# Kernel optimization log

Measured on AMD Instinct MI355X. Metric: run time of the kernel, lower is better.

## Reference

```python
import jax, jax.numpy as jnp
import numpy as np

_COOR = [[1,4],[1,5],[1,6],[2,4],[2,6],[3,1],[3,2],[3,3],[3,4],[3,5],[3,6],[3,7],[3,8],[3,9],[4,1],[4,2],[4,3],[4,4],[4,5],[4,6],[4,7],[4,8],[4,9],[5,1],[5,2],[5,3],[5,4],[5,5],[5,6],[5,7],[5,8],[5,9],[6,1],[6,2],[6,3],[6,4],[6,5],[6,6],[6,7],[6,8],[6,9],[7,1],[7,2],[7,3],[7,4],[7,5],[7,6],[7,7],[7,8],[7,9],[8,2],[8,3],[8,4],[8,5],[8,6],[8,7],[8,8],[9,3],[9,4],[9,5],[9,6],[9,7]]
_DIRS = [[1,2,3,4,5,6,7,8,9,10,11,12,13,14,15,16,17,18,19,20,21,22,23,24,25,26,27,28,29,30,31,32,33,34,35,36,37,38,39,40,41,42,43,44,45,46,47,48,49,50,58,52,53,54,55,56,62,60,61,51,57,59],[59,57,51,61,60,62,56,55,54,53,52,58,50,41,32,23,14,49,40,31,22,13,48,39,30,21,12,47,38,29,20,11,46,37,28,19,10,45,36,27,18,9,44,35,26,17,8,43,34,25,16,7,42,33,24,15,6,5,4,3,2,1],[59,57,51,61,60,62,56,55,54,53,52,58,50,49,48,47,46,45,44,43,42,41,40,39,38,37,36,35,34,33,32,31,30,29,28,27,26,25,24,23,22,21,20,19,18,17,16,15,14,13,12,11,10,9,8,7,6,5,4,3,2,1],[1,2,3,4,5,6,15,24,33,42,7,16,25,34,43,8,17,26,35,44,9,18,27,36,45,10,19,28,37,46,11,20,29,38,47,12,21,30,39,48,13,22,31,40,49,14,23,32,41,50,58,52,53,54,55,56,62,60,61,51,57,59]]


def _build_graph():
    D, E = len(_DIRS), len(_COOR)
    Ns = np.zeros((D, E, E), np.float32)
    for di, direction in enumerate(_DIRS):
        for pi in range(E):
            i, j = _COOR[direction[pi] - 1]
            nbrs = {0: [[i, j - 1], [i - 1, j - 1], [i - 1, j]],
                    1: [[i, j + 1], [i - 1, j], [i - 1, j + 1]],
                    2: [[i, j - 1], [i + 1, j - 1], [i + 1, j]],
                    3: [[i, j - 1], [i - 1, j - 1], [i - 1, j]]}[di]
            for nb in nbrs:
                if nb in _COOR:
                    n_idx = _COOR.index(nb) + 1
                    if n_idx in direction[:pi]:
                        Ns[di, pi, direction.index(n_idx)] = 1.0
    perm = np.asarray(_DIRS, np.int32) - 1  # [D,E] electrode index visited at each step
    return jnp.asarray(Ns), jnp.asarray(perm)


def _srnn(x_t, Ns, perm, U_w, U_b, W_w, W_b, sp_bs, P_w, P_b, ps_w, ps_b):
    # x_t: [B,E,C] -> m: [B,HID]
    B, E, _ = x_t.shape
    HID = U_b.shape[1]

    def one_dir(ns, pm, uw, ub, ww, wb, b, pw, pb):
        ux = jnp.einsum('bec,hc->beh', x_t[:, pm], uw) + ub  # [B,E,H] precomputed input term
        H0 = jnp.zeros((B, E, ub.shape[0]), x_t.dtype)

        def step(H, inp):
            ns_row, ux_pi, pi = inp
            # ns_row is nonzero only at already-visited step positions (< pi)
            h_agg = jnp.einsum('e,beh->bh', ns_row, H)
            h = jax.nn.relu(ux_pi + h_agg @ ww.T + wb + b)
            return jax.lax.dynamic_update_slice(H, h[:, None, :], (0, pi, 0)), None

        H, _ = jax.lax.scan(step, H0, (ns, jnp.swapaxes(ux, 0, 1), jnp.arange(E)))
        return jnp.einsum('beh,pe->bhp', H, pw) + pb  # [B,H,P]

    s = jax.vmap(one_dir)(Ns, perm, U_w, U_b, W_w, W_b, sp_bs, P_w, P_b)  # [D,B,H,P]
    s = jnp.moveaxis(s, 0, 2).reshape(B, HID, -1)  # [B,H,D*P]
    return (s @ ps_w.T + ps_b)[..., 0]  # [B,H]


def _trnn(ms, rs_w, rs_b, vs_w, vs_b, bs, pj_w, pj_b):
    # ms: [T,B,H]
    h0 = jnp.zeros(ms.shape[1:], ms.dtype)

    def step(h, m_t):
        h = jax.nn.relu(m_t @ rs_w.T + rs_b + h @ vs_w.T + vs_b + bs)
        return h, h

    _, hs = jax.lax.scan(step, h0, ms)  # [T,B,H]
    return jnp.einsum('tbh,pt->bph', hs, pj_w) + pj_b[None, :, None]  # [B,P,H]


def _forward(x, Ns, perm, U_w, U_b, W_w, W_b, sp_bs, P_w, P_b, ps_w, ps_b,
             f_rs_w, f_rs_b, f_vs_w, f_vs_b, f_bs, f_pj_w, f_pj_b,
             b_rs_w, b_rs_b, b_vs_w, b_vs_b, b_bs, b_pj_w, b_pj_b,
             fp1_w, fp1_b, fp2_w, fp2_b, bp1_w, bp1_b, bp2_w, bp2_b):
    xt = jnp.swapaxes(x, 0, 1)  # [T,B,E,C]
    ms = jax.vmap(lambda xi: _srnn(xi, Ns, perm, U_w, U_b, W_w, W_b, sp_bs,
                                   P_w, P_b, ps_w, ps_b))(xt)  # [T,B,H]
    q_f = _trnn(ms, f_rs_w, f_rs_b, f_vs_w, f_vs_b, f_bs, f_pj_w, f_pj_b)
    q_b = _trnn(ms[::-1], b_rs_w, b_rs_b, b_vs_w, b_vs_b, b_bs, b_pj_w, b_pj_b)
    zf = (q_f @ fp1_w.T + fp1_b)[..., 0]  # [B,Ptp]
    zb = (q_b @ bp1_w.T + bp1_b)[..., 0]
    return zf @ fp2_w.T + fp2_b + zb @ bp2_w.T + bp2_b  # [B,classes]


def setup_inputs() -> dict:
    B, T, E, C = 128, 16, 62, 5
    HID, SPP, TPP, NC, D = 128, 16, 8, 3, 4
    Ns, perm = _build_graph()
    key = jax.random.key(0)
    ks = jax.random.split(key, 34)
    rnd = lambda k, s: (jax.random.normal(k, s, jnp.float32) * 0.05)
    return {
        'x': jax.random.normal(ks[0], (B, T, E, C), jnp.float32),
        'Ns': Ns, 'perm': perm,
        'U_w': rnd(ks[1], (D, HID, C)), 'U_b': rnd(ks[2], (D, HID)),
        'W_w': rnd(ks[3], (D, HID, HID)), 'W_b': rnd(ks[4], (D, HID)),
        'sp_bs': rnd(ks[5], (D, HID)),
        'P_w': rnd(ks[6], (D, SPP, E)), 'P_b': rnd(ks[7], (D, SPP)),
        'ps_w': rnd(ks[8], (1, D * SPP)), 'ps_b': rnd(ks[9], (1,)),
        'f_rs_w': rnd(ks[10], (HID, HID)), 'f_rs_b': rnd(ks[11], (HID,)),
        'f_vs_w': rnd(ks[12], (HID, HID)), 'f_vs_b': rnd(ks[13], (HID,)),
        'f_bs': rnd(ks[14], (HID,)),
        'f_pj_w': rnd(ks[15], (TPP, T)), 'f_pj_b': rnd(ks[16], (TPP,)),
        'b_rs_w': rnd(ks[17], (HID, HID)), 'b_rs_b': rnd(ks[18], (HID,)),
        'b_vs_w': rnd(ks[19], (HID, HID)), 'b_vs_b': rnd(ks[20], (HID,)),
        'b_bs': rnd(ks[21], (HID,)),
        'b_pj_w': rnd(ks[22], (TPP, T)), 'b_pj_b': rnd(ks[23], (TPP,)),
        'fp1_w': rnd(ks[24], (1, HID)), 'fp1_b': rnd(ks[25], (1,)),
        'fp2_w': rnd(ks[26], (NC, TPP)), 'fp2_b': rnd(ks[27], (NC,)),
        'bp1_w': rnd(ks[28], (1, HID)), 'bp1_b': rnd(ks[29], (1,)),
        'bp2_w': rnd(ks[30], (NC, TPP)), 'bp2_b': rnd(ks[31], (NC,)),
    }


def reference(x, Ns, perm, U_w, U_b, W_w, W_b, sp_bs, P_w, P_b, ps_w, ps_b,
              f_rs_w, f_rs_b, f_vs_w, f_vs_b, f_bs, f_pj_w, f_pj_b,
              b_rs_w, b_rs_b, b_vs_w, b_vs_b, b_bs, b_pj_w, b_pj_b,
              fp1_w, fp1_b, fp2_w, fp2_b, bp1_w, bp1_b, bp2_w, bp2_b):
    return _forward(x, Ns, perm, U_w, U_b, W_w, W_b, sp_bs, P_w, P_b, ps_w, ps_b,
                    f_rs_w, f_rs_b, f_vs_w, f_vs_b, f_bs, f_pj_w, f_pj_b,
                    b_rs_w, b_rs_b, b_vs_w, b_vs_b, b_bs, b_pj_w, b_pj_b,
                    fp1_w, fp1_b, fp2_w, fp2_b, bp1_w, bp1_b, bp2_w, bp2_b)
```

## Files before the change

kernel.cpp:

```cpp
#include <hip/hip_runtime.h>
#include <utility>

typedef unsigned short u16;
typedef unsigned int   u32;

using bf16x8 = __attribute__((ext_vector_type(8))) short;
using f32x4  = __attribute__((ext_vector_type(4))) float;
using u32x4  = __attribute__((ext_vector_type(4))) unsigned;

__device__ __forceinline__ u32 cvtpk(float lo, float hi) {
  u32 r;
  asm("v_cvt_pk_bf16_f32 %0, %1, %2" : "=v"(r) : "v"(lo), "v"(hi));
  return r;
}
__device__ __forceinline__ bf16x8 pack8(float f0,float f1,float f2,float f3,
                                        float f4,float f5,float f6,float f7) {
  u32x4 t; t[0]=cvtpk(f0,f1); t[1]=cvtpk(f2,f3); t[2]=cvtpk(f4,f5); t[3]=cvtpk(f6,f7);
  return __builtin_bit_cast(bf16x8, t);
}
__device__ __forceinline__ u16 f2bf(float f) {
  u32 u = __float_as_uint(f);
  u32 r = u + 0x7FFFu + ((u >> 16) & 1u);
  return (u16)(r >> 16);
}

struct Sched {
  unsigned v[4][64];
  unsigned char opi[4][64];
  int nslot;
};

constexpr int cCOOR[62][2] = {
  {1,4},{1,5},{1,6},{2,4},{2,6},
  {3,1},{3,2},{3,3},{3,4},{3,5},{3,6},{3,7},{3,8},{3,9},
  {4,1},{4,2},{4,3},{4,4},{4,5},{4,6},{4,7},{4,8},{4,9},
  {5,1},{5,2},{5,3},{5,4},{5,5},{5,6},{5,7},{5,8},{5,9},
  {6,1},{6,2},{6,3},{6,4},{6,5},{6,6},{6,7},{6,8},{6,9},
  {7,1},{7,2},{7,3},{7,4},{7,5},{7,6},{7,7},{7,8},{7,9},
  {8,2},{8,3},{8,4},{8,5},{8,6},{8,7},{8,8},
  {9,3},{9,4},{9,5},{9,6},{9,7}};

constexpr int cDIRS[4][62] = {
  {1,2,3,4,5,6,7,8,9,10,11,12,13,14,15,16,17,18,19,20,21,22,23,24,25,26,27,28,29,30,
   31,32,33,34,35,36,37,38,39,40,41,42,43,44,45,46,47,48,49,50,
   58,52,53,54,55,56,62,60,61,51,57,59},
  {59,57,51,61,60,62,56,55,54,53,52,58,50,41,32,23,14,49,40,31,22,13,48,39,30,21,12,
   47,38,29,20,11,46,37,28,19,10,45,36,27,18,9,44,35,26,17,8,43,34,25,16,7,42,33,24,
   15,6,5,4,3,2,1},
  {59,57,51,61,60,62,56,55,54,53,52,58,50,49,48,47,46,45,44,43,42,41,40,39,38,37,36,
   35,34,33,32,31,30,29,28,27,26,25,24,23,22,21,20,19,18,17,16,15,14,13,12,11,10,9,
   8,7,6,5,4,3,2,1},
  {1,2,3,4,5,6,15,24,33,42,7,16,25,34,43,8,17,26,35,44,9,18,27,36,45,10,19,28,37,46,
   11,20,29,38,47,12,21,30,39,48,13,22,31,40,49,14,23,32,41,50,
   58,52,53,54,55,56,62,60,61,51,57,59}};

constexpr int cOFFS[4][3][2] = {
  {{0,-1},{-1,-1},{-1,0}},
  {{0, 1},{-1, 0},{-1,1}},
  {{0,-1},{ 1,-1},{ 1,0}},
  {{0,-1},{-1,-1},{-1,0}}};

constexpr Sched make_sched() {
  Sched S{};
  int nslot_all = 0;
  for (int d = 0; d < 4; ++d) {
    int pos_of[63] = {};
    for (int p = 0; p < 62; ++p) pos_of[cDIRS[d][p]] = p;
    int nb[62][3] = {}; int nc[62] = {}; int rdcnt[62] = {};
    for (int p = 0; p < 62; ++p) {
      const int e = cDIRS[d][p];
      const int ci = cCOOR[e-1][0], cj = cCOOR[e-1][1];
      for (int o = 0; o < 3; ++o) {
        const int ni = ci + cOFFS[d][o][0], nj = cj + cOFFS[d][o][1];
        int q = 0;
        for (int k2 = 0; k2 < 62; ++k2)
          if (cCOOR[k2][0]==ni && cCOOR[k2][1]==nj) { q = k2+1; break; }
        if (q) { const int qp = pos_of[q];
          if (qp < p) { nb[p][nc[p]] = qp; nc[p] = nc[p]+1; rdcnt[qp] = rdcnt[qp]+1; } }
      }
    }
    int lvl[62] = {};
    for (int p = 0; p < 62; ++p) {
      int m = 0;
      for (int o = 0; o < nc[p]; ++o) if (lvl[nb[p][o]] > m) m = lvl[nb[p][o]];
      lvl[p] = m + 1;
    }
    int ord[62] = {}; int k = 0;
    for (int L = 1; L <= 62; ++L)
      for (int p = 0; p < 62; ++p) if (lvl[p] == L) { ord[k] = p; k = k+1; }
    int slotof[62] = {};
    int rl[20]; int lr[20];
    for (int s = 0; s < 20; ++s) { rl[s] = 0; lr[s] = -1; }
    int nslot = 0, cur_sub = 0;
    int barafter[62] = {};
    int prev_lvl = lvl[ord[0]];
    for (int kk = 0; kk < 62; ++kk) {
      const int p = ord[kk];
      if (lvl[p] != prev_lvl) { barafter[kk-1] = 1; cur_sub = cur_sub+1; prev_lvl = lvl[p]; }
      for (int o = 0; o < nc[p]; ++o) {
        const int s = slotof[nb[p][o]];
        rl[s] = rl[s]-1;
        if (cur_sub > lr[s]) lr[s] = cur_sub;
      }
      int myslot = 31;
      if (rdcnt[p] > 0) {
        int found = -1;
        for (int s = 0; s < nslot; ++s)
          if (rl[s] == 0 && lr[s] < cur_sub) { found = s; break; }
        if (found < 0 && nslot < 19) { found = nslot; nslot = nslot+1; }
        if (found < 0) {
          barafter[kk-1] = 1; cur_sub = cur_sub+1;
          for (int o = 0; o < nc[p]; ++o) {
            const int s = slotof[nb[p][o]];
            if (cur_sub > lr[s]) lr[s] = cur_sub;
          }
          for (int s = 0; s < nslot; ++s)
            if (rl[s] == 0 && lr[s] < cur_sub) { found = s; break; }
        }
        if (found < 0 && nslot < 20) { found = nslot; nslot = nslot+1; }
        if (found < 0) found = 0;
        myslot = found;
        rl[myslot] = rdcnt[p];
        lr[myslot] = -1;
        slotof[p] = myslot;
      }
      S.opi[d][kk] = (unsigned char)p;
      S.v[d][kk] = (unsigned)(cDIRS[d][p]-1)
                 | ((unsigned)myslot << 6)
                 | ((unsigned)nc[p] << 11)
                 | ((unsigned)(nc[p]>0 ? slotof[nb[p][0]] : 0) << 13)
                 | ((unsigned)(nc[p]>1 ? slotof[nb[p][1]] : 0) << 18)
                 | ((unsigned)(nc[p]>2 ? slotof[nb[p][2]] : 0) << 23);
    }
    for (int kk = 0; kk < 62; ++kk) if (barafter[kk]) S.v[d][kk] |= (1u << 28);
    if (nslot > nslot_all) nslot_all = nslot;
  }
  S.nslot = nslot_all;
  return S;
}

constexpr Sched g_sched = make_sched();
static_assert(g_sched.nslot >= 8 && g_sched.nslot <= 20, "slot pressure out of range");
__constant__ Sched c_sched = make_sched();

constexpr int POOL_B    = g_sched.nslot * 4096;
constexpr int SRNN_SMEM = POOL_B + 256;

template <int D, int K>
__device__ __forceinline__ void do_step(
    char* smem, const float* s_wp,
    const bf16x8 (&wf)[2][4], const bf16x8& uwf0, const bf16x8& uwf1,
    float bias0, float bias1,
    const u32 (&xr)[16][3], const int (&bad)[4],
    const u32 (&rdv)[4], const u32 (&wav)[4],
    f32x4& macc0, f32x4& macc1)
{
  constexpr unsigned sv = g_sched.v[D][K];
  constexpr int snew = (int)((sv >> 6) & 31u);
  constexpr int nbc  = (int)((sv >> 11) & 3u);
  constexpr int sl0  = (int)((sv >> 13) & 31u);
  constexpr int sl1  = (int)((sv >> 18) & 31u);
  constexpr int sl2  = (int)((sv >> 23) & 31u);
  constexpr int g    = K & 3;
  constexpr int js   = K >> 2;

  u32 r0 = (u32)__builtin_amdgcn_ds_bpermute(bad[g], (int)xr[js][0]);
  u32 r1 = (u32)__builtin_amdgcn_ds_bpermute(bad[g], (int)xr[js][1]);
  u32 r2 = (u32)__builtin_amdgcn_ds_bpermute(bad[g], (int)xr[js][2]);

  f32x4 a0 = {bias0, bias0, bias0, bias0};
  f32x4 a1 = {bias1, bias1, bias1, bias1};

  if constexpr (nbc > 0) {
#pragma unroll
    for (int kc = 0; kc < 4; ++kc) {
      bf16x8 a = *(const bf16x8*)(smem + sl0 * 4096 + rdv[kc]);
      a0 = __builtin_amdgcn_mfma_f32_16x16x32_bf16(a, wf[0][kc], a0, 0, 0, 0);
      a1 = __builtin_amdgcn_mfma_f32_16x16x32_bf16(a, wf[1][kc], a1, 0, 0, 0);
    }
  }
  if constexpr (nbc > 1) {
#pragma unroll
    for (int kc = 0; kc < 4; ++kc) {
      bf16x8 a = *(const bf16x8*)(smem + sl1 * 4096 + rdv[kc]);
      a0 = __builtin_amdgcn_mfma_f32_16x16x32_bf16(a, wf[0][kc], a0, 0, 0, 0);
      a1 = __builtin_amdgcn_mfma_f32_16x16x32_bf16(a, wf[1][kc], a1, 0, 0, 0);
    }
  }
  if constexpr (nbc > 2) {
#pragma unroll
    for (int kc = 0; kc < 4; ++kc) {
      bf16x8 a = *(const bf16x8*)(smem + sl2 * 4096 + rdv[kc]);
      a0 = __builtin_amdgcn_mfma_f32_16x16x32_bf16(a, wf[0][kc], a0, 0, 0, 0);
      a1 = __builtin_amdgcn_mfma_f32_16x16x32_bf16(a, wf[1][kc], a1, 0, 0, 0);
    }
  }
  {
    u32x4 xv; xv[0] = r0; xv[1] = r1; xv[2] = r2; xv[3] = 0;
    bf16x8 xa = __builtin_bit_cast(bf16x8, xv);
    a0 = __builtin_amdgcn_mfma_f32_16x16x32_bf16(xa, uwf0, a0, 0, 0, 0);
    a1 = __builtin_amdgcn_mfma_f32_16x16x32_bf16(xa, uwf1, a1, 0, 0, 0);
  }

  const float wp = s_wp[K];
  float h0[4], h1[4];
#pragma unroll
  for (int r = 0; r < 4; ++r) { h0[r] = fmaxf(a0[r], 0.f); h1[r] = fmaxf(a1[r], 0.f); }
  if constexpr (snew != 31) {
#pragma unroll
    for (int r = 0; r < 4; ++r)
      *(u32*)(smem + snew * 4096 + wav[r]) = cvtpk(h0[r], h1[r]);
  }
#pragma unroll
  for (int r = 0; r < 4; ++r) { macc0[r] += h0[r] * wp; macc1[r] += h1[r] * wp; }

  if constexpr ((sv >> 28) & 1u) __syncthreads();
}

template <int D, int... Ks>
__device__ __forceinline__ void run_steps(
    std::integer_sequence<int, Ks...>,
    char* smem, const float* s_wp,
    const bf16x8 (&wf)[2][4], const bf16x8& uwf0, const bf16x8& uwf1,
    float bias0, float bias1,
    const u32 (&xr)[16][3], const int (&bad)[4],
    const u32 (&rdv)[4], const u32 (&wav)[4],
    f32x4& macc0, f32x4& macc1)
{
  (do_step<D, Ks>(smem, s_wp, wf, uwf0, uwf1, bias0, bias1,
                  xr, bad, rdv, wav, macc0, macc1), ...);
}

template <int D>
__device__ __noinline__ void srnn_body(
    const float* __restrict__ x,  const float* __restrict__ Uw,
    const float* __restrict__ Ub, const float* __restrict__ Ww,
    const float* __restrict__ Wb, const float* __restrict__ spbs,
    const float* __restrict__ Pw, const float* __restrict__ psw,
    float* __restrict__ part, int bx)
{
  extern __shared__ __align__(16) char smem[];
  const int tid  = threadIdx.x;
  const int lane = tid & 63, wid = tid >> 6;
  const int l15  = lane & 15, lhi = lane >> 4;
  const int bb = bx & 15, tp = bx >> 6;
  const int b0 = bb * 8, t0 = tp * 2;

  float* s_wp = (float*)(smem + POOL_B);

  if (tid < 62) {
    const int opi = c_sched.opi[D][tid];
    float acc = 0.f;
    for (int q = 0; q < 16; ++q) acc += Pw[(D * 16 + q) * 62 + opi] * psw[D * 16 + q];
    s_wp[tid] = acc;
  }

  bf16x8 wf[2][4];
  float bias0, bias1;
#pragma unroll
  for (int nt = 0; nt < 2; ++nt) {
    const int n = wid * 32 + nt * 16 + l15;
    const float* wr = Ww + (size_t)(D * 128 + n) * 128;
#pragma unroll
    for (int kc = 0; kc < 4; ++kc) {
      float4 lo = *(const float4*)(wr + kc * 32 + lhi * 4);
      float4 hi = *(const float4*)(wr + kc * 32 + lhi * 4 + 16);
      wf[nt][kc] = pack8(lo.x, hi.x, lo.y, hi.y, lo.z, hi.z, lo.w, hi.w);
    }
    float bnt = Ub[D * 128 + n] + Wb[D * 128 + n] + spbs[D * 128 + n];
    if (nt == 0) bias0 = bnt; else bias1 = bnt;
  }

  float u0a=0,u1a=0,u2a=0,u3a=0,u4a=0, u0b=0,u1b=0,u2b=0,u3b=0,u4b=0;
  if (lhi == 0) {
    const float* ua = Uw + (D * 128 + wid * 32 + l15) * 5;
    const float* ub = Uw + (D * 128 + wid * 32 + 16 + l15) * 5;
    u0a=ua[0]; u1a=ua[1]; u2a=ua[2]; u3a=ua[3]; u4a=ua[4];
    u0b=ub[0]; u1b=ub[1]; u2b=ub[2]; u3b=ub[3]; u4b=ub[4];
  }
  const bf16x8 uwf0 = pack8(u0a,u1a,u2a,u3a,u4a,0.f,0.f,0.f);
  const bf16x8 uwf1 = pack8(u0b,u1b,u2b,u3b,u4b,0.f,0.f,0.f);

  const float* xlane = x + (size_t)((b0 + (l15 & 7)) * 16 + (t0 + (l15 >> 3))) * 310;
  u32 xr[16][3];
#pragma unroll
  for (int j = 0; j < 16; ++j) {
    const int e = (int)(c_sched.v[D][j * 4 + lhi] & 63u);
    const float* xp = xlane + e * 5;
    float x0 = xp[0], x1 = xp[1], x2 = xp[2], x3 = xp[3], x4 = xp[4];
    xr[j][0] = cvtpk(x0, x1);
    xr[j][1] = cvtpk(x2, x3);
    xr[j][2] = cvtpk(x4, 0.f);
  }

  const int swz_r = ((l15 & 7) << 4);
  u32 rdv[4], wav[4];
#pragma unroll
  for (int kc = 0; kc < 4; ++kc)
    rdv[kc] = (u32)(l15 * 256 + ((kc * 64 + lhi * 16) ^ swz_r));
  const int wcol = wid * 64 + l15 * 4;
#pragma unroll
  for (int r = 0; r < 4; ++r) {
    const int row = lhi * 4 + r;
    wav[r] = (u32)(row * 256 + (wcol ^ ((row & 7) << 4)));
  }
  int bad[4];
#pragma unroll
  for (int i = 0; i < 4; ++i) bad[i] = (i * 16 + l15) * 4;

  __syncthreads();

  f32x4 macc0 = {0.f,0.f,0.f,0.f}, macc1 = {0.f,0.f,0.f,0.f};
  run_steps<D>(std::make_integer_sequence<int, 62>{},
               smem, s_wp, wf, uwf0, uwf1, bias0, bias1,
               xr, bad, rdv, wav, macc0, macc1);

#pragma unroll
  for (int r = 0; r < 4; ++r) {
    const int row = lhi * 4 + r;
    const int t = t0 + (row >> 3);
    const int brow = b0 + (row & 7);
    const int n0 = wid * 32 + l15;
    float* pp = part + (((size_t)D * 16 + t) * 128 + brow) * 128;
    pp[n0]      = macc0[r];
    pp[n0 + 16] = macc1[r];
  }
}

__global__ __launch_bounds__(256, 2) void srnn_kernel(
    const float* __restrict__ x,  const float* __restrict__ Uw,
    const float* __restrict__ Ub, const float* __restrict__ Ww,
    const float* __restrict__ Wb, const float* __restrict__ spbs,
    const float* __restrict__ Pw, const float* __restrict__ psw,
    float* __restrict__ part)
{
  const int bx = blockIdx.x;
  switch ((bx >> 4) & 3) {
    case 0: srnn_body<0>(x, Uw, Ub, Ww, Wb, spbs, Pw, psw, part, bx); break;
    case 1: srnn_body<1>(x, Uw, Ub, Ww, Wb, spbs, Pw, psw, part, bx); break;
    case 2: srnn_body<2>(x, Uw, Ub, Ww, Wb, spbs, Pw, psw, part, bx); break;
    default: srnn_body<3>(x, Uw, Ub, Ww, Wb, spbs, Pw, psw, part, bx); break;
  }
}

__global__ __launch_bounds__(256) void reduce_ms_kernel(
    const float* __restrict__ part, const float* __restrict__ Pb,
    const float* __restrict__ psw,  const float* __restrict__ psb,
    u16* __restrict__ msbf, float* __restrict__ out)
{
  const int tid = threadIdx.x;
  if (blockIdx.x == 0 && tid < 128) {
    float3 z = {0.f, 0.f, 0.f};
    *(float3*)(out + tid * 3) = z;
  }
  const int idx = blockIdx.x * 256 + tid;
  float c0 = psb[0];
  for (int i = 0; i < 64; ++i) c0 += Pb[i] * psw[i];
  float s = c0 + part[idx] + part[262144 + idx] + part[2 * 262144 + idx] + part[3 * 262144 + idx];
  msbf[idx] = f2bf(s);
}

constexpr int MS_OFF = 0;
constexpr int HB_OFF = 65536;
constexpr int SW_OFF = HB_OFF + 8704;
constexpr int S2_OFF = SW_OFF + 4096;
constexpr int TRNN_SMEM = S2_OFF + 1024;

__global__ __launch_bounds__(256) void trnn_kernel(
    const u16* __restrict__ msbf,
    const float* __restrict__ frs, const float* __restrict__ frsb,
    const float* __restrict__ fvs, const float* __restrict__ fvsb,
    const float* __restrict__ fbs, const float* __restrict__ fpj, const float* __restrict__ fpjb,
    const float* __restrict__ brs, const float* __restrict__ brsb,
    const float* __restrict__ bvs, const float* __restrict__ bvsb,
    const float* __restrict__ bbs, const float* __restrict__ bpj, const float* __restrict__ bpjb,
    const float* __restrict__ fp1w, const float* __restrict__ fp1b,
    const float* __restrict__ fp2w, const float* __restrict__ fp2b,
    const float* __restrict__ bp1w, const float* __restrict__ bp1b,
    const float* __restrict__ bp2w, const float* __restrict__ bp2b,
    float* __restrict__ out)
{
  extern __shared__ __align__(16) char smem[];
  const int tid = threadIdx.x;
  const int lane = tid & 63, wid = tid >> 6;
  const int l15 = lane & 15, lhi = lane >> 4;
  const int dir = blockIdx.x & 1;
  const int b0 = (blockIdx.x >> 1) * 16;

  const float* rs  = dir ? brs  : frs;
  const float* rsb = dir ? brsb : frsb;
  const float* vs  = dir ? bvs  : fvs;
  const float* vsb = dir ? bvsb : fvsb;
  const float* bs  = dir ? bbs  : fbs;
  const float* w1  = dir ? bp1w : fp1w;

  {
    const int tq = tid >> 4, bq = tid & 15;
    const u16* mg = msbf + ((size_t)tq * 128 + b0 + bq) * 128;
    char* mrow = smem + MS_OFF + (tq * 16 + bq) * 256;
    const int sz = (bq & 7) << 4;
#pragma unroll
    for (int q = 0; q < 16; ++q) {
      uint4 v = *(const uint4*)(mg + q * 8);
      *(u32*)(mrow + ((q * 16)      ^ sz)) = v.x;
      *(u32*)(mrow + ((q * 16 + 4)  ^ sz)) = v.y;
      *(u32*)(mrow + ((q * 16 + 8)  ^ sz)) = v.z;
      *(u32*)(mrow + ((q * 16 + 12) ^ sz)) = v.w;
    }
  }

  bf16x8 rf[2][4], vf[2][4];
  float bias[2], w1a, w1b;
#pragma unroll
  for (int nt = 0; nt < 2; ++nt) {
    const int n = wid * 32 + nt * 16 + l15;
#pragma unroll
    for (int kc = 0; kc < 4; ++kc) {
      float4 ra = *(const float4*)(rs + (size_t)n * 128 + kc * 32 + lhi * 8);
      float4 rb = *(const float4*)(rs + (size_t)n * 128 + kc * 32 + lhi * 8 + 4);
      rf[nt][kc] = pack8(ra.x, ra.y, ra.z, ra.w, rb.x, rb.y, rb.z, rb.w);
      float4 lo = *(const float4*)(vs + (size_t)n * 128 + kc * 32 + lhi * 4);
      float4 hi = *(const float4*)(vs + (size_t)n * 128 + kc * 32 + lhi * 4 + 16);
      vf[nt][kc] = pack8(lo.x, hi.x, lo.y, hi.y, lo.z, hi.z, lo.w, hi.w);
    }
    bias[nt] = rsb[n] + vsb[n] + bs[n];
  }
  w1a = w1[wid * 32 + l15];
  w1b = w1[wid * 32 + 16 + l15];

  for (int i = tid; i < 2176; i += 256) *(u16*)(smem + HB_OFF + i * 2) = 0;
  __syncthreads();

  float* sredw = (float*)(smem + SW_OFF);
  float* sred2 = (float*)(smem + S2_OFF);

  int cur = 0;
  for (int tt2 = 0; tt2 < 16; ++tt2) {
    const int tt = dir ? (15 - tt2) : tt2;
    f32x4 am0 = {bias[0],bias[0],bias[0],bias[0]};
    f32x4 am1 = {bias[1],bias[1],bias[1],bias[1]};
    f32x4 ah0 = {0.f,0.f,0.f,0.f}, ah1 = {0.f,0.f,0.f,0.f};
    const char* msrow = smem + MS_OFF + (tt * 16 + l15) * 256;
    const int msz = (l15 & 7) << 4;
#pragma unroll
    for (int kc = 0; kc < 4; ++kc) {
      bf16x8 ma = *(const bf16x8*)(msrow + ((kc * 64 + lhi * 16) ^ msz));
      bf16x8 ha = *(const bf16x8*)(smem + HB_OFF + (cur * 16 + l15) * 272 + kc * 64 + lhi * 16);
      am0 = __builtin_amdgcn_mfma_f32_16x16x32_bf16(ma, rf[0][kc], am0, 0, 0, 0);
      ah0 = __builtin_amdgcn_mfma_f32_16x16x32_bf16(ha, vf[0][kc], ah0, 0, 0, 0);
      am1 = __builtin_amdgcn_mfma_f32_16x16x32_bf16(ma, rf[1][kc], am1, 0, 0, 0);
      ah1 = __builtin_amdgcn_mfma_f32_16x16x32_bf16(ha, vf[1][kc], ah1, 0, 0, 0);
    }
    float pr[4];
#pragma unroll
    for (int r = 0; r < 4; ++r) {
      const int row = lhi * 4 + r;
      float h0 = fmaxf(am0[r] + ah0[r], 0.f);
      float h1 = fmaxf(am1[r] + ah1[r], 0.f);
      *(u32*)(smem + HB_OFF + ((cur ^ 1) * 16 + row) * 272 + wid * 64 + l15 * 4) = cvtpk(h0, h1);
      pr[r] = h0 * w1a + h1 * w1b;
    }
#pragma unroll
    for (int r = 0; r < 4; ++r) {
      float p = pr[r];
      p += __shfl_xor(p, 1);
      p += __shfl_xor(p, 2);
      p += __shfl_xor(p, 4);
      p += __shfl_xor(p, 8);
      if (l15 == 0) sredw[(tt2 * 16 + lhi * 4 + r) * 4 + wid] = p;
    }
    __syncthreads();
    cur ^= 1;
  }

  {
    const int tq = tid >> 4, bq = tid & 15;
    const float* sw = sredw + (tq * 16 + bq) * 4;
    sred2[tq * 16 + bq] = sw[0] + sw[1] + sw[2] + sw[3];
  }
  __syncthreads();

  if (tid < 48) {
    const int b = tid / 3, c = tid % 3;
    const float* p1w = dir ? bp1w : fp1w;
    const float* p1b = dir ? bp1b : fp1b;
    const float* p2w = dir ? bp2w : fp2w;
    const float* p2b = dir ? bp2b : fp2b;
    const float* pj  = dir ? bpj  : fpj;
    const float* pjb = dir ? bpjb : fpjb;
    float S1 = 0.f;
    for (int h = 0; h < 128; ++h) S1 += p1w[h];
    float val = p2b[c];
    for (int p = 0; p < 8; ++p) val += (pjb[p] * S1 + p1b[0]) * p2w[c * 8 + p];
    for (int t2 = 0; t2 < 16; ++t2) {
      float g = 0.f;
      for (int p = 0; p < 8; ++p) g += p2w[c * 8 + p] * pj[p * 16 + t2];
      val += sred2[t2 * 16 + b] * g;
    }
    atomicAdd(out + (b0 + b) * 3 + c, val);
  }
}

extern "C" void kernel_launch(void* const* d_in, const int* in_sizes, int n_in,
                              void* d_out, int out_size, void* d_ws, size_t ws_size,
                              hipStream_t stream)
{
  (void)in_sizes; (void)n_in; (void)out_size; (void)ws_size;
  const float* x    = (const float*)d_in[0];
  const float* Uw   = (const float*)d_in[3];
  const float* Ub   = (const float*)d_in[4];
  const float* Ww   = (const float*)d_in[5];
  const float* Wb   = (const float*)d_in[6];
  const float* spbs = (const float*)d_in[7];
  const float* Pw   = (const float*)d_in[8];
  const float* Pb   = (const float*)d_in[9];
  const float* psw  = (const float*)d_in[10];
  const float* psb  = (const float*)d_in[11];
  const float* frs  = (const float*)d_in[12];
  const float* frsb = (const float*)d_in[13];
  const float* fvs  = (const float*)d_in[14];
  const float* fvsb = (const float*)d_in[15];
  const float* fbs  = (const float*)d_in[16];
  const float* fpj  = (const float*)d_in[17];
  const float* fpjb = (const float*)d_in[18];
  const float* brs  = (const float*)d_in[19];
  const float* brsb = (const float*)d_in[20];
  const float* bvs  = (const float*)d_in[21];
  const float* bvsb = (const float*)d_in[22];
  const float* bbs  = (const float*)d_in[23];
  const float* bpj  = (const float*)d_in[24];
  const float* bpjb = (const float*)d_in[25];
  const float* fp1w = (const float*)d_in[26];
  const float* fp1b = (const float*)d_in[27];
  const float* fp2w = (const float*)d_in[28];
  const float* fp2b = (const float*)d_in[29];
  const float* bp1w = (const float*)d_in[30];
  const float* bp1b = (const float*)d_in[31];
  const float* bp2w = (const float*)d_in[32];
  const float* bp2b = (const float*)d_in[33];

  char* ws = (char*)d_ws;
  float* part = (float*)ws;
  u16*   msbf = (u16*)(ws + 4194304);

  hipFuncSetAttribute((const void*)srnn_kernel,
                      hipFuncAttributeMaxDynamicSharedMemorySize, SRNN_SMEM);
  hipFuncSetAttribute((const void*)trnn_kernel,
                      hipFuncAttributeMaxDynamicSharedMemorySize, TRNN_SMEM);

  srnn_kernel<<<dim3(512), dim3(256), SRNN_SMEM, stream>>>(
      x, Uw, Ub, Ww, Wb, spbs, Pw, psw, part);
  reduce_ms_kernel<<<dim3(1024), dim3(256), 0, stream>>>(
      part, Pb, psw, psb, msbf, (float*)d_out);
  trnn_kernel<<<dim3(16), dim3(256), TRNN_SMEM, stream>>>(msbf,
      frs, frsb, fvs, fvsb, fbs, fpj, fpjb,
      brs, brsb, bvs, bvsb, bbs, bpj, bpjb,
      fp1w, fp1b, fp2w, fp2b, bp1w, bp1b, bp2w, bp2b,
      (float*)d_out);
}
```

Measured before the change: 76.31 us.

## Replace fully unrolled per-direction recurrence with runtime phase loop and LDS prefetch

Drops the four template-instantiated, fully unrolled 62-step recurrence bodies. A single kernel body now walks a constexpr phase table at runtime, double-buffering the neighbour hidden-state LDS reads and the x loads one step ahead of the MFMA compute. x is read from global per step instead of being preloaded into registers and shuffled with bpermute. This shrinks code size and register pressure, at the cost of runtime branching on schedule bits, dynamic slot addressing, and a global load on every step.

```diff
diff --git a/kernel.cpp b/kernel.cpp
--- a/kernel.cpp
+++ b/kernel.cpp
@@ -1,5 +1,4 @@
 #include <hip/hip_runtime.h>
-#include <utility>
 
 typedef unsigned short u16;
 typedef unsigned int   u32;
@@ -27,7 +26,11 @@
 struct Sched {
   unsigned v[4][64];
   unsigned char opi[4][64];
+  unsigned char ph_start[4][32];
+  unsigned char ph_len[4][32];
+  int nph[4];
   int nslot;
+  int maxph;
 };
 
 constexpr int cCOOR[62][2] = {
@@ -62,7 +65,7 @@
 
 constexpr Sched make_sched() {
   Sched S{};
-  int nslot_all = 0;
+  int nslot_all = 0, maxph_all = 0;
   for (int d = 0; d < 4; ++d) {
     int pos_of[63] = {};
     for (int p = 0; p < 62; ++p) pos_of[cDIRS[d][p]] = p;
@@ -132,200 +135,31 @@
                  | ((unsigned)(nc[p]>1 ? slotof[nb[p][1]] : 0) << 18)
                  | ((unsigned)(nc[p]>2 ? slotof[nb[p][2]] : 0) << 23);
     }
-    for (int kk = 0; kk < 62; ++kk) if (barafter[kk]) S.v[d][kk] |= (1u << 28);
+    int np = 0, st = 0;
+    for (int kk = 0; kk < 62; ++kk) {
+      if (barafter[kk] || kk == 61) {
+        S.ph_start[d][np] = (unsigned char)st;
+        S.ph_len[d][np]   = (unsigned char)(kk - st + 1);
+        np = np + 1;
+        st = kk + 1;
+      }
+    }
+    S.nph[d] = np;
+    if (np > maxph_all) maxph_all = np;
     if (nslot > nslot_all) nslot_all = nslot;
   }
   S.nslot = nslot_all;
+  S.maxph = maxph_all;
   return S;
 }
 
 constexpr Sched g_sched = make_sched();
 static_assert(g_sched.nslot >= 8 && g_sched.nslot <= 20, "slot pressure out of range");
+static_assert(g_sched.maxph <= 32, "phase table overflow");
 __constant__ Sched c_sched = make_sched();
 
 constexpr int POOL_B    = g_sched.nslot * 4096;
 constexpr int SRNN_SMEM = POOL_B + 256;
-
-template <int D, int K>
-__device__ __forceinline__ void do_step(
-    char* smem, const float* s_wp,
-    const bf16x8 (&wf)[2][4], const bf16x8& uwf0, const bf16x8& uwf1,
-    float bias0, float bias1,
-    const u32 (&xr)[16][3], const int (&bad)[4],
-    const u32 (&rdv)[4], const u32 (&wav)[4],
-    f32x4& macc0, f32x4& macc1)
-{
-  constexpr unsigned sv = g_sched.v[D][K];
-  constexpr int snew = (int)((sv >> 6) & 31u);
-  constexpr int nbc  = (int)((sv >> 11) & 3u);
-  constexpr int sl0  = (int)((sv >> 13) & 31u);
-  constexpr int sl1  = (int)((sv >> 18) & 31u);
-  constexpr int sl2  = (int)((sv >> 23) & 31u);
-  constexpr int g    = K & 3;
-  constexpr int js   = K >> 2;
-
-  u32 r0 = (u32)__builtin_amdgcn_ds_bpermute(bad[g], (int)xr[js][0]);
-  u32 r1 = (u32)__builtin_amdgcn_ds_bpermute(bad[g], (int)xr[js][1]);
-  u32 r2 = (u32)__builtin_amdgcn_ds_bpermute(bad[g], (int)xr[js][2]);
-
-  f32x4 a0 = {bias0, bias0, bias0, bias0};
-  f32x4 a1 = {bias1, bias1, bias1, bias1};
-
-  if constexpr (nbc > 0) {
-#pragma unroll
-    for (int kc = 0; kc < 4; ++kc) {
-      bf16x8 a = *(const bf16x8*)(smem + sl0 * 4096 + rdv[kc]);
-      a0 = __builtin_amdgcn_mfma_f32_16x16x32_bf16(a, wf[0][kc], a0, 0, 0, 0);
-      a1 = __builtin_amdgcn_mfma_f32_16x16x32_bf16(a, wf[1][kc], a1, 0, 0, 0);
-    }
-  }
-  if constexpr (nbc > 1) {
-#pragma unroll
-    for (int kc = 0; kc < 4; ++kc) {
-      bf16x8 a = *(const bf16x8*)(smem + sl1 * 4096 + rdv[kc]);
-      a0 = __builtin_amdgcn_mfma_f32_16x16x32_bf16(a, wf[0][kc], a0, 0, 0, 0);
-      a1 = __builtin_amdgcn_mfma_f32_16x16x32_bf16(a, wf[1][kc], a1, 0, 0, 0);
-    }
-  }
-  if constexpr (nbc > 2) {
-#pragma unroll
-    for (int kc = 0; kc < 4; ++kc) {
-      bf16x8 a = *(const bf16x8*)(smem + sl2 * 4096 + rdv[kc]);
-      a0 = __builtin_amdgcn_mfma_f32_16x16x32_bf16(a, wf[0][kc], a0, 0, 0, 0);
-      a1 = __builtin_amdgcn_mfma_f32_16x16x32_bf16(a, wf[1][kc], a1, 0, 0, 0);
-    }
-  }
-  {
-    u32x4 xv; xv[0] = r0; xv[1] = r1; xv[2] = r2; xv[3] = 0;
-    bf16x8 xa = __builtin_bit_cast(bf16x8, xv);
-    a0 = __builtin_amdgcn_mfma_f32_16x16x32_bf16(xa, uwf0, a0, 0, 0, 0);
-    a1 = __builtin_amdgcn_mfma_f32_16x16x32_bf16(xa, uwf1, a1, 0, 0, 0);
-  }
-
-  const float wp = s_wp[K];
-  float h0[4], h1[4];
-#pragma unroll
-  for (int r = 0; r < 4; ++r) { h0[r] = fmaxf(a0[r], 0.f); h1[r] = fmaxf(a1[r], 0.f); }
-  if constexpr (snew != 31) {
-#pragma unroll
-    for (int r = 0; r < 4; ++r)
-      *(u32*)(smem + snew * 4096 + wav[r]) = cvtpk(h0[r], h1[r]);
-  }
-#pragma unroll
-  for (int r = 0; r < 4; ++r) { macc0[r] += h0[r] * wp; macc1[r] += h1[r] * wp; }
-
-  if constexpr ((sv >> 28) & 1u) __syncthreads();
-}
-
-template <int D, int... Ks>
-__device__ __forceinline__ void run_steps(
-    std::integer_sequence<int, Ks...>,
-    char* smem, const float* s_wp,
-    const bf16x8 (&wf)[2][4], const bf16x8& uwf0, const bf16x8& uwf1,
-    float bias0, float bias1,
-    const u32 (&xr)[16][3], const int (&bad)[4],
-    const u32 (&rdv)[4], const u32 (&wav)[4],
-    f32x4& macc0, f32x4& macc1)
-{
-  (do_step<D, Ks>(smem, s_wp, wf, uwf0, uwf1, bias0, bias1,
-                  xr, bad, rdv, wav, macc0, macc1), ...);
-}
-
-template <int D>
-__device__ __noinline__ void srnn_body(
-    const float* __restrict__ x,  const float* __restrict__ Uw,
-    const float* __restrict__ Ub, const float* __restrict__ Ww,
-    const float* __restrict__ Wb, const float* __restrict__ spbs,
-    const float* __restrict__ Pw, const float* __restrict__ psw,
-    float* __restrict__ part, int bx)
-{
-  extern __shared__ __align__(16) char smem[];
-  const int tid  = threadIdx.x;
-  const int lane = tid & 63, wid = tid >> 6;
-  const int l15  = lane & 15, lhi = lane >> 4;
-  const int bb = bx & 15, tp = bx >> 6;
-  const int b0 = bb * 8, t0 = tp * 2;
-
-  float* s_wp = (float*)(smem + POOL_B);
-
-  if (tid < 62) {
-    const int opi = c_sched.opi[D][tid];
-    float acc = 0.f;
-    for (int q = 0; q < 16; ++q) acc += Pw[(D * 16 + q) * 62 + opi] * psw[D * 16 + q];
-    s_wp[tid] = acc;
-  }
-
-  bf16x8 wf[2][4];
-  float bias0, bias1;
-#pragma unroll
-  for (int nt = 0; nt < 2; ++nt) {
-    const int n = wid * 32 + nt * 16 + l15;
-    const float* wr = Ww + (size_t)(D * 128 + n) * 128;
-#pragma unroll
-    for (int kc = 0; kc < 4; ++kc) {
-      float4 lo = *(const float4*)(wr + kc * 32 + lhi * 4);
-      float4 hi = *(const float4*)(wr + kc * 32 + lhi * 4 + 16);
-      wf[nt][kc] = pack8(lo.x, hi.x, lo.y, hi.y, lo.z, hi.z, lo.w, hi.w);
-    }
-    float bnt = Ub[D * 128 + n] + Wb[D * 128 + n] + spbs[D * 128 + n];
-    if (nt == 0) bias0 = bnt; else bias1 = bnt;
-  }
-
-  float u0a=0,u1a=0,u2a=0,u3a=0,u4a=0, u0b=0,u1b=0,u2b=0,u3b=0,u4b=0;
-  if (lhi == 0) {
-    const float* ua = Uw + (D * 128 + wid * 32 + l15) * 5;
-    const float* ub = Uw + (D * 128 + wid * 32 + 16 + l15) * 5;
-    u0a=ua[0]; u1a=ua[1]; u2a=ua[2]; u3a=ua[3]; u4a=ua[4];
-    u0b=ub[0]; u1b=ub[1]; u2b=ub[2]; u3b=ub[3]; u4b=ub[4];
-  }
-  const bf16x8 uwf0 = pack8(u0a,u1a,u2a,u3a,u4a,0.f,0.f,0.f);
-  const bf16x8 uwf1 = pack8(u0b,u1b,u2b,u3b,u4b,0.f,0.f,0.f);
-
-  const float* xlane = x + (size_t)((b0 + (l15 & 7)) * 16 + (t0 + (l15 >> 3))) * 310;
-  u32 xr[16][3];
-#pragma unroll
-  for (int j = 0; j < 16; ++j) {
-    const int e = (int)(c_sched.v[D][j * 4 + lhi] & 63u);
-    const float* xp = xlane + e * 5;
-    float x0 = xp[0], x1 = xp[1], x2 = xp[2], x3 = xp[3], x4 = xp[4];
-    xr[j][0] = cvtpk(x0, x1);
-    xr[j][1] = cvtpk(x2, x3);
-    xr[j][2] = cvtpk(x4, 0.f);
-  }
-
-  const int swz_r = ((l15 & 7) << 4);
-  u32 rdv[4], wav[4];
-#pragma unroll
-  for (int kc = 0; kc < 4; ++kc)
-    rdv[kc] = (u32)(l15 * 256 + ((kc * 64 + lhi * 16) ^ swz_r));
-  const int wcol = wid * 64 + l15 * 4;
-#pragma unroll
-  for (int r = 0; r < 4; ++r) {
-    const int row = lhi * 4 + r;
-    wav[r] = (u32)(row * 256 + (wcol ^ ((row & 7) << 4)));
-  }
-  int bad[4];
-#pragma unroll
-  for (int i = 0; i < 4; ++i) bad[i] = (i * 16 + l15) * 4;
-
-  __syncthreads();
-
-  f32x4 macc0 = {0.f,0.f,0.f,0.f}, macc1 = {0.f,0.f,0.f,0.f};
-  run_steps<D>(std::make_integer_sequence<int, 62>{},
-               smem, s_wp, wf, uwf0, uwf1, bias0, bias1,
-               xr, bad, rdv, wav, macc0, macc1);
-
-#pragma unroll
-  for (int r = 0; r < 4; ++r) {
-    const int row = lhi * 4 + r;
-    const int t = t0 + (row >> 3);
-    const int brow = b0 + (row & 7);
-    const int n0 = wid * 32 + l15;
-    float* pp = part + (((size_t)D * 16 + t) * 128 + brow) * 128;
-    pp[n0]      = macc0[r];
-    pp[n0 + 16] = macc1[r];
-  }
-}
 
 __global__ __launch_bounds__(256, 2) void srnn_kernel(
     const float* __restrict__ x,  const float* __restrict__ Uw,
@@ -334,12 +168,169 @@
     const float* __restrict__ Pw, const float* __restrict__ psw,
     float* __restrict__ part)
 {
+  extern __shared__ __align__(16) char smem[];
+  const int tid  = threadIdx.x;
+  const int lane = tid & 63, wid = tid >> 6;
+  const int l15  = lane & 15, lhi = lane >> 4;
   const int bx = blockIdx.x;
-  switch ((bx >> 4) & 3) {
-    case 0: srnn_body<0>(x, Uw, Ub, Ww, Wb, spbs, Pw, psw, part, bx); break;
-    case 1: srnn_body<1>(x, Uw, Ub, Ww, Wb, spbs, Pw, psw, part, bx); break;
-    case 2: srnn_body<2>(x, Uw, Ub, Ww, Wb, spbs, Pw, psw, part, bx); break;
-    default: srnn_body<3>(x, Uw, Ub, Ww, Wb, spbs, Pw, psw, part, bx); break;
+  const int bb = bx & 15, d = (bx >> 4) & 3, tp = bx >> 6;
+  const int b0 = bb * 8, t0 = tp * 2;
+
+  float* s_wp = (float*)(smem + POOL_B);
+
+  if (tid < 62) {
+    const int opi = c_sched.opi[d][tid];
+    float acc = 0.f;
+    for (int q = 0; q < 16; ++q) acc += Pw[(d * 16 + q) * 62 + opi] * psw[d * 16 + q];
+    s_wp[tid] = acc;
+  }
+
+  bf16x8 wf[2][4];
+  float bias0, bias1;
+#pragma unroll
+  for (int nt = 0; nt < 2; ++nt) {
+    const int n = wid * 32 + nt * 16 + l15;
+    const float* wr = Ww + (size_t)(d * 128 + n) * 128;
+#pragma unroll
+    for (int kc = 0; kc < 4; ++kc) {
+      float4 lo = *(const float4*)(wr + kc * 32 + lhi * 4);
+      float4 hi = *(const float4*)(wr + kc * 32 + lhi * 4 + 16);
+      wf[nt][kc] = pack8(lo.x, hi.x, lo.y, hi.y, lo.z, hi.z, lo.w, hi.w);
+    }
+    float bnt = Ub[d * 128 + n] + Wb[d * 128 + n] + spbs[d * 128 + n];
+    if (nt == 0) bias0 = bnt; else bias1 = bnt;
+  }
+
+  float u0a=0,u1a=0,u2a=0,u3a=0,u4a=0, u0b=0,u1b=0,u2b=0,u3b=0,u4b=0;
+  if (lhi == 0) {
+    const float* ua = Uw + (d * 128 + wid * 32 + l15) * 5;
+    const float* ub = Uw + (d * 128 + wid * 32 + 16 + l15) * 5;
+    u0a=ua[0]; u1a=ua[1]; u2a=ua[2]; u3a=ua[3]; u4a=ua[4];
+    u0b=ub[0]; u1b=ub[1]; u2b=ub[2]; u3b=ub[3]; u4b=ub[4];
+  }
+  const bf16x8 uwf0 = pack8(u0a,u1a,u2a,u3a,u4a,0.f,0.f,0.f);
+  const bf16x8 uwf1 = pack8(u0b,u1b,u2b,u3b,u4b,0.f,0.f,0.f);
+
+  const int swz_r = ((l15 & 7) << 4);
+  u32 rdv[4], wav[4];
+#pragma unroll
+  for (int kc = 0; kc < 4; ++kc)
+    rdv[kc] = (u32)(l15 * 256 + ((kc * 64 + lhi * 16) ^ swz_r));
+  const int wcol = wid * 64 + l15 * 4;
+#pragma unroll
+  for (int r = 0; r < 4; ++r) {
+    const int row = lhi * 4 + r;
+    wav[r] = (u32)(row * 256 + (wcol ^ ((row & 7) << 4)));
+  }
+
+  const float* xlane = x + (size_t)((b0 + (l15 & 7)) * 16 + (t0 + (l15 >> 3))) * 310;
+  const unsigned* scv = c_sched.v[d];
+
+  f32x4 macc0 = {0.f,0.f,0.f,0.f}, macc1 = {0.f,0.f,0.f,0.f};
+
+  auto prefetch = [&](unsigned sv, bf16x8 (&A0)[4], bf16x8 (&A1)[4], float (&xv)[5]) {
+    const char* p0 = smem + ((sv >> 13) & 31u) * 4096;
+    const char* p1 = smem + ((sv >> 18) & 31u) * 4096;
+#pragma unroll
+    for (int kc = 0; kc < 4; ++kc) {
+      A0[kc] = *(const bf16x8*)(p0 + rdv[kc]);
+      A1[kc] = *(const bf16x8*)(p1 + rdv[kc]);
+    }
+    float x0=0,x1=0,x2=0,x3=0,x4=0;
+    if (lhi == 0) {
+      const float* xp = xlane + (sv & 63u) * 5;
+      x0=xp[0]; x1=xp[1]; x2=xp[2]; x3=xp[3]; x4=xp[4];
+    }
+    xv[0]=x0; xv[1]=x1; xv[2]=x2; xv[3]=x3; xv[4]=x4;
+  };
+
+  auto compute = [&](unsigned sv, int kidx,
+                     const bf16x8 (&A0)[4], const bf16x8 (&A1)[4], const float (&xv)[5]) {
+    const int nbc = (int)((sv >> 11) & 3u);
+    bf16x8 C2[4];
+    if (nbc > 2) {
+      const char* p2 = smem + ((sv >> 23) & 31u) * 4096;
+#pragma unroll
+      for (int kc = 0; kc < 4; ++kc) C2[kc] = *(const bf16x8*)(p2 + rdv[kc]);
+    }
+    f32x4 a0 = {bias0, bias0, bias0, bias0};
+    f32x4 a1 = {bias1, bias1, bias1, bias1};
+    if (nbc > 0) {
+#pragma unroll
+      for (int kc = 0; kc < 4; ++kc) {
+        a0 = __builtin_amdgcn_mfma_f32_16x16x32_bf16(A0[kc], wf[0][kc], a0, 0, 0, 0);
+        a1 = __builtin_amdgcn_mfma_f32_16x16x32_bf16(A0[kc], wf[1][kc], a1, 0, 0, 0);
+      }
+    }
+    if (nbc > 1) {
+#pragma unroll
+      for (int kc = 0; kc < 4; ++kc) {
+        a0 = __builtin_amdgcn_mfma_f32_16x16x32_bf16(A1[kc], wf[0][kc], a0, 0, 0, 0);
+        a1 = __builtin_amdgcn_mfma_f32_16x16x32_bf16(A1[kc], wf[1][kc], a1, 0, 0, 0);
+      }
+    }
+    if (nbc > 2) {
+#pragma unroll
+      for (int kc = 0; kc < 4; ++kc) {
+        a0 = __builtin_amdgcn_mfma_f32_16x16x32_bf16(C2[kc], wf[0][kc], a0, 0, 0, 0);
+        a1 = __builtin_amdgcn_mfma_f32_16x16x32_bf16(C2[kc], wf[1][kc], a1, 0, 0, 0);
+      }
+    }
+    bf16x8 xa = pack8(xv[0], xv[1], xv[2], xv[3], xv[4], 0.f, 0.f, 0.f);
+    a0 = __builtin_amdgcn_mfma_f32_16x16x32_bf16(xa, uwf0, a0, 0, 0, 0);
+    a1 = __builtin_amdgcn_mfma_f32_16x16x32_bf16(xa, uwf1, a1, 0, 0, 0);
+
+    const int snew = (int)((sv >> 6) & 31u);
+    const float wp = s_wp[kidx];
+    float h0r[4], h1r[4];
+#pragma unroll
+    for (int r = 0; r < 4; ++r) { h0r[r] = fmaxf(a0[r], 0.f); h1r[r] = fmaxf(a1[r], 0.f); }
+    if (snew != 31) {
+      char* dst = smem + snew * 4096;
+#pragma unroll
+      for (int r = 0; r < 4; ++r)
+        *(u32*)(dst + wav[r]) = cvtpk(h0r[r], h1r[r]);
+    }
+#pragma unroll
+    for (int r = 0; r < 4; ++r) { macc0[r] += h0r[r] * wp; macc1[r] += h1r[r] * wp; }
+  };
+
+  __syncthreads();
+
+  bf16x8 PA[4], PB[4], QA[4], QB[4];
+  float pxv[5], qxv[5];
+
+  const int nph = c_sched.nph[d];
+  int s = 0;
+  for (int ph = 0; ph < nph; ++ph) {
+    int rem = (int)c_sched.ph_len[d][ph];
+    prefetch(scv[s], PA, PB, pxv);
+    while (rem >= 2) {
+      prefetch(scv[s + 1], QA, QB, qxv);
+      compute(scv[s], s, PA, PB, pxv);
+      ++s; --rem;
+      if (rem >= 2) {
+        prefetch(scv[s + 1], PA, PB, pxv);
+        compute(scv[s], s, QA, QB, qxv);
+        ++s; --rem;
+      } else {
+        compute(scv[s], s, QA, QB, qxv);
+        ++s; --rem;
+      }
+    }
+    if (rem == 1) { compute(scv[s], s, PA, PB, pxv); ++s; }
+    __syncthreads();
+  }
+
+#pragma unroll
+  for (int r = 0; r < 4; ++r) {
+    const int row = lhi * 4 + r;
+    const int t = t0 + (row >> 3);
+    const int brow = b0 + (row & 7);
+    const int n0 = wid * 32 + l15;
+    float* pp = part + (((size_t)d * 16 + t) * 128 + brow) * 128;
+    pp[n0]      = macc0[r];
+    pp[n0 + 16] = macc1[r];
   }
 }
 
```

After: 79.58 us. +4.3%, slower.
